# Kernel optimization log

Measured on AMD Instinct MI355X. Metric: run time of the kernel, lower is better.

Reference implementation:

```python
import jax, jax.numpy as jnp
import numpy as np

D_MODEL = 2048
NUM_HEADS = 16
HEAD_DIM = D_MODEL // NUM_HEADS
BATCH = 2
SEQ = 2048
ROPE_BASE = 10000.0


def apply_rope(x, start_pos=0):
    # x: [B, H, S, D] ; standard rotate-half RoPE
    B, H, S, D = x.shape
    inv_freq = 1.0 / (ROPE_BASE ** (jnp.arange(0, D, 2, dtype=jnp.float32) / D))  # [D/2]
    pos = jnp.arange(start_pos, start_pos + S, dtype=jnp.float32)  # [S]
    ang = pos[:, None] * inv_freq[None, :]  # [S, D/2]
    cos = jnp.cos(ang).astype(x.dtype)
    sin = jnp.sin(ang).astype(x.dtype)
    x1, x2 = x[..., : D // 2], x[..., D // 2 :]
    return jnp.concatenate([x1 * cos - x2 * sin, x1 * sin + x2 * cos], axis=-1)


def setup_inputs() -> dict:
    key = jax.random.key(0)
    ks = jax.random.split(key, 9)
    s = 1.0 / np.sqrt(D_MODEL)
    inp = {
        "x": jax.random.normal(ks[0], (BATCH, SEQ, D_MODEL), dtype=jnp.float32),
        "mask": jnp.tril(jnp.ones((SEQ, SEQ), dtype=jnp.float32)),  # causal
        "Wq_w": jax.random.normal(ks[1], (D_MODEL, D_MODEL), dtype=jnp.float32) * s,
        "Wq_b": jax.random.normal(ks[2], (D_MODEL,), dtype=jnp.float32) * 0.01,
        "Wk_w": jax.random.normal(ks[3], (D_MODEL, D_MODEL), dtype=jnp.float32) * s,
        "Wk_b": jax.random.normal(ks[4], (D_MODEL,), dtype=jnp.float32) * 0.01,
        "Wv_w": jax.random.normal(ks[5], (D_MODEL, D_MODEL), dtype=jnp.float32) * s,
        "Wv_b": jax.random.normal(ks[6], (D_MODEL,), dtype=jnp.float32) * 0.01,
        "Wo_w": jax.random.normal(ks[7], (D_MODEL, D_MODEL), dtype=jnp.float32) * s,
        "Wo_b": jax.random.normal(ks[8], (D_MODEL,), dtype=jnp.float32) * 0.01,
    }
    return inp


def reference(x, mask, Wq_w, Wq_b, Wk_w, Wk_b, Wv_w, Wv_b, Wo_w, Wo_b):
    B, S, _ = x.shape
    # projections (torch Linear: y = x @ W.T + b)
    Q = x @ Wq_w.T + Wq_b
    K = x @ Wk_w.T + Wk_b
    V = x @ Wv_w.T + Wv_b
    # [B, H, S, D]
    Q = Q.reshape(B, S, NUM_HEADS, HEAD_DIM).transpose(0, 2, 1, 3)
    K = K.reshape(B, S, NUM_HEADS, HEAD_DIM).transpose(0, 2, 1, 3)
    V = V.reshape(B, S, NUM_HEADS, HEAD_DIM).transpose(0, 2, 1, 3)
    Q = apply_rope(Q, start_pos=0)
    K = apply_rope(K, start_pos=0)
    scores = jnp.einsum("bhqd,bhkd->bhqk", Q, K) / jnp.sqrt(
        jnp.asarray(HEAD_DIM, dtype=x.dtype)
    )
    # 2-D mask -> broadcast over batch/head; masked_fill(mask==0, -inf)
    scores = jnp.where(mask[None, None, :S, :S] == 0, -jnp.inf, scores)
    attn = jax.nn.softmax(scores, axis=-1)
    out = jnp.einsum("bhqk,bhkd->bhqd", attn, V)
    out = out.transpose(0, 2, 1, 3).reshape(B, S, D_MODEL)
    return out @ Wo_w.T + Wo_b
```

## Files before the change

kernel.cpp:

```cpp
#include <hip/hip_runtime.h>
#include <math.h>

#define D_MODEL 2048
#define NHEADS  16
#define HDIM    128
#define BATCH   2
#define SEQ     2048
#define MTOT    (BATCH*SEQ)

typedef unsigned short u16;
typedef unsigned int   u32;
typedef __attribute__((ext_vector_type(8))) short  short8;
typedef __attribute__((ext_vector_type(8))) u16    ushort8;
typedef __attribute__((ext_vector_type(4))) u16    us4;
typedef __attribute__((ext_vector_type(4))) float  floatx4;

__device__ __forceinline__ u16 f2b(float f) {
    u32 u = __float_as_uint(f);
    return (u16)((u + 0x7fffu + ((u >> 16) & 1u)) >> 16);
}
__device__ __forceinline__ float b2f(u16 b) {
    return __uint_as_float(((u32)b) << 16);
}
__device__ __forceinline__ void async16(void* lds, const void* g) {
    __builtin_amdgcn_global_load_lds(
        (const __attribute__((address_space(1))) u32*)g,
        (__attribute__((address_space(3))) u32*)lds, 16, 0, 0);
}

__global__ __launch_bounds__(256)
void f2b_kernel(const float* __restrict__ x,
                const float* __restrict__ wq, const float* __restrict__ wk,
                const float* __restrict__ wv, const float* __restrict__ wo,
                u16* __restrict__ xb, u16* __restrict__ wqb, u16* __restrict__ wkb,
                u16* __restrict__ wvb, u16* __restrict__ wob)
{
    const int bid = blockIdx.x;
    const float* src; u16* dst; int lb;
    if (bid < 4096) { src = x; dst = xb; lb = bid; }
    else {
        const int t = (bid - 4096) >> 11;
        lb = (bid - 4096) & 2047;
        src = (t == 0) ? wq : (t == 1) ? wk : (t == 2) ? wv : wo;
        dst = (t == 0) ? wqb : (t == 1) ? wkb : (t == 2) ? wvb : wob;
    }
    const size_t e = ((size_t)lb * 256 + threadIdx.x) * 8;
    const float4 a = *(const float4*)&src[e];
    const float4 b = *(const float4*)&src[e + 4];
    union { u16 u[8]; uint4 v; } o;
    o.u[0] = f2b(a.x); o.u[1] = f2b(a.y); o.u[2] = f2b(a.z); o.u[3] = f2b(a.w);
    o.u[4] = f2b(b.x); o.u[5] = f2b(b.y); o.u[6] = f2b(b.z); o.u[7] = f2b(b.w);
    *(uint4*)&dst[e] = o.v;
}

__global__ __launch_bounds__(256)
void gemm_bf16(const u16* __restrict__ A,
               const u16* W0, const u16* W1, const u16* W2,
               const float* b0, const float* b1, const float* b2,
               void* C0, void* C1, void* C2, int mode)
{
    __shared__ __align__(16) u16 As[128 * 32];
    __shared__ __align__(16) u16 Bs[128 * 32];

    const int z = blockIdx.z;
    const u16*   W    = (z == 0) ? W0 : (z == 1) ? W1 : W2;
    const float* bias = (z == 0) ? b0 : (z == 1) ? b1 : b2;
    void*        C    = (z == 0) ? C0 : (z == 1) ? C1 : C2;

    const int tid  = threadIdx.x;
    const int lane = tid & 63;
    const int wv   = tid >> 6;
    const int wr   = wv >> 1, wc = wv & 1;
    const int m0 = blockIdx.y * 128, n0 = blockIdx.x * 128;

    floatx4 acc[4][4];
    #pragma unroll
    for (int i = 0; i < 4; ++i)
        #pragma unroll
        for (int j = 0; j < 4; ++j) acc[i][j] = (floatx4){0.f, 0.f, 0.f, 0.f};

    const int f0 = tid, f1 = tid + 256;
    const char* Ag = (const char*)(A + (size_t)m0 * 2048);
    const char* Wg = (const char*)(W + (size_t)n0 * 2048);
    const size_t a0 = (size_t)(f0 >> 2) * 4096 + (f0 & 3) * 16;
    const size_t a1 = (size_t)(f1 >> 2) * 4096 + (f1 & 3) * 16;

    const int lrow = lane & 15, lk = (lane >> 4) * 8;

    for (int k0 = 0; k0 < 2048; k0 += 32) {
        __syncthreads();
        const size_t kb = (size_t)k0 * 2;
        async16(&As[f0 * 8], Ag + a0 + kb);
        async16(&As[f1 * 8], Ag + a1 + kb);
        async16(&Bs[f0 * 8], Wg + a0 + kb);
        async16(&Bs[f1 * 8], Wg + a1 + kb);
        __syncthreads();

        short8 af[4], bf[4];
        #pragma unroll
        for (int i = 0; i < 4; ++i)
            af[i] = *(const short8*)&As[(wr * 64 + i * 16 + lrow) * 32 + lk];
        #pragma unroll
        for (int j = 0; j < 4; ++j)
            bf[j] = *(const short8*)&Bs[(wc * 64 + j * 16 + lrow) * 32 + lk];
        #pragma unroll
        for (int i = 0; i < 4; ++i)
            #pragma unroll
            for (int j = 0; j < 4; ++j)
                acc[i][j] = __builtin_amdgcn_mfma_f32_16x16x32_bf16(af[i], bf[j], acc[i][j], 0, 0, 0);
    }

    float bb[4];
    #pragma unroll
    for (int j = 0; j < 4; ++j) bb[j] = bias[n0 + wc * 64 + j * 16 + lrow];

    #pragma unroll
    for (int i = 0; i < 4; ++i) {
        #pragma unroll
        for (int j = 0; j < 4; ++j) {
            const int col  = n0 + wc * 64 + j * 16 + lrow;
            const int row0 = m0 + wr * 64 + i * 16 + (lane >> 4) * 4;
            if (mode == 0) {
                const int b = row0 >> 11, s = row0 & (SEQ - 1);
                const int h = col >> 7,  d = col & 127;
                if (z == 2) {
                    us4 pk;
                    #pragma unroll
                    for (int q = 0; q < 4; ++q) pk[q] = f2b(acc[i][j][q] + bb[j]);
                    *(us4*)&((u16*)C)[(((size_t)(b * NHEADS + h)) * HDIM + d) * SEQ + s] = pk;
                } else {
                    #pragma unroll
                    for (int q = 0; q < 4; ++q)
                        ((u16*)C)[(((size_t)(b * NHEADS + h)) * SEQ + s + q) * HDIM + d]
                            = f2b(acc[i][j][q] + bb[j]);
                }
            } else {
                #pragma unroll
                for (int q = 0; q < 4; ++q)
                    ((float*)C)[(size_t)(row0 + q) * D_MODEL + col] = acc[i][j][q] + bb[j];
            }
        }
    }
}

__global__ void rope_table(float* __restrict__ tcos, float* __restrict__ tsin)
{
    const int idx = blockIdx.x * 256 + threadIdx.x;
    const int s = idx >> 6, i = idx & 63;
    const float inv = powf(10000.0f, -(float)i / 64.0f);
    const float ang = (float)s * inv;
    tcos[idx] = cosf(ang);
    tsin[idx] = sinf(ang);
}

__global__ void rope_apply(u16* __restrict__ Q, u16* __restrict__ K,
                           const float* __restrict__ tcos, const float* __restrict__ tsin)
{
    const int idx = blockIdx.x * 256 + threadIdx.x;
    u16* P = blockIdx.y ? K : Q;
    const float sc = blockIdx.y ? 1.0f : 0.08838834764831845f;
    const int i   = idx & 63;
    const int bhs = idx >> 6;
    const int s   = bhs & (SEQ - 1);
    const size_t base = (size_t)bhs * HDIM;
    const float x1 = b2f(P[base + i]), x2 = b2f(P[base + i + 64]);
    const float c  = tcos[(s << 6) + i], sn = tsin[(s << 6) + i];
    P[base + i]      = f2b((x1 * c  - x2 * sn) * sc);
    P[base + i + 64] = f2b((x1 * sn + x2 * c) * sc);
}

__global__ __launch_bounds__(256, 2)
void flash_attn_mfma(const u16* __restrict__ Q, const u16* __restrict__ K,
                     const u16* __restrict__ Vt, u16* __restrict__ O)
{
    __shared__ __align__(16) u16 Ks[2][64 * 128];
    __shared__ __align__(16) u16 Vs[2][128 * 64];
    __shared__ __align__(16) u16 Ps[128 * 64];

    const int tid = threadIdx.x, lane = tid & 63, w = tid >> 6;
    const int l15 = lane & 15, l4 = lane >> 4;
    const int bh = blockIdx.y;
    const int qt = 15 - blockIdx.x;
    const int q0 = qt * 128;
    const int qw = q0 + w * 32;
    const size_t baseQK = (size_t)bh * SEQ * HDIM;
    const size_t baseV  = (size_t)bh * HDIM * SEQ;

    short8 qf[2][4];
    #pragma unroll
    for (int u = 0; u < 2; ++u) {
        const u16* Qg = Q + baseQK + (size_t)(qw + u * 16 + l15) * HDIM;
        #pragma unroll
        for (int kk = 0; kk < 4; ++kk) qf[u][kk] = *(const short8*)&Qg[kk * 32 + l4 * 8];
    }

    floatx4 o_acc[2][8];
    #pragma unroll
    for (int u = 0; u < 2; ++u)
        #pragma unroll
        for (int j2 = 0; j2 < 8; ++j2) o_acc[u][j2] = (floatx4){0.f, 0.f, 0.f, 0.f};
    float m_run[2] = {-INFINITY, -INFINITY}, l_run[2] = {0.f, 0.f};

    const int nt = 2 * qt + 2;

    #define STAGE(buf, k0_)                                                     \
    {                                                                           \
        const u16* Kg = K  + baseQK + (size_t)(k0_) * HDIM;                     \
        const u16* Vg = Vt + baseV  + (k0_);                                    \
        _Pragma("unroll")                                                       \
        for (int p_ = 0; p_ < 4; ++p_) {                                        \
            const int idx = p_ * 256 + tid;                                     \
            const int r_ = idx >> 4, c_ = idx & 15;                             \
            const int srcK = (c_ & 8) | ((c_ & 7) ^ (r_ & 7));                  \
            async16(&Ks[buf][idx * 8], Kg + r_ * HDIM + srcK * 8);              \
            const int rv = idx >> 3, cv = idx & 7;                              \
            const int srcV = cv ^ (rv & 7);                                     \
            async16(&Vs[buf][idx * 8], Vg + (size_t)rv * SEQ + srcV * 8);       \
        }                                                                       \
    }

    STAGE(0, 0);
    __syncthreads();
    int cur = 0;

    for (int t = 0; t < nt; ++t) {
        if (t + 1 < nt) STAGE(cur ^ 1, (t + 1) * 64);

        floatx4 s[2][4];
        #pragma unroll
        for (int u = 0; u < 2; ++u)
            #pragma unroll
            for (int j = 0; j < 4; ++j) s[u][j] = (floatx4){0.f, 0.f, 0.f, 0.f};
        #pragma unroll
        for (int j = 0; j < 4; ++j) {
            const int row = j * 16 + l15;
            #pragma unroll
            for (int kk = 0; kk < 4; ++kk) {
                const int x  = kk * 4 + l4;
                const int ch = (x & 8) | ((x & 7) ^ (row & 7));
                const short8 kf = *(const short8*)&Ks[cur][row * 128 + ch * 8];
                s[0][j] = __builtin_amdgcn_mfma_f32_16x16x32_bf16(kf, qf[0][kk], s[0][j], 0, 0, 0);
                s[1][j] = __builtin_amdgcn_mfma_f32_16x16x32_bf16(kf, qf[1][kk], s[1][j], 0, 0, 0);
            }
        }

        if (t >= nt - 2) {
            const int k0 = t * 64;
            #pragma unroll
            for (int u = 0; u < 2; ++u) {
                const int qg = qw + u * 16 + l15;
                #pragma unroll
                for (int j = 0; j < 4; ++j)
                    #pragma unroll
                    for (int r = 0; r < 4; ++r)
                        if (k0 + j * 16 + l4 * 4 + r > qg) s[u][j][r] = -INFINITY;
            }
        }

        float al[2];
        #pragma unroll
        for (int u = 0; u < 2; ++u) {
            float m0_ = fmaxf(fmaxf(s[u][0][0], s[u][0][1]), fmaxf(s[u][0][2], s[u][0][3]));
            float m1_ = fmaxf(fmaxf(s[u][1][0], s[u][1][1]), fmaxf(s[u][1][2], s[u][1][3]));
            float m2_ = fmaxf(fmaxf(s[u][2][0], s[u][2][1]), fmaxf(s[u][2][2], s[u][2][3]));
            float m3_ = fmaxf(fmaxf(s[u][3][0], s[u][3][1]), fmaxf(s[u][3][2], s[u][3][3]));
            float mt = fmaxf(fmaxf(m0_, m1_), fmaxf(m2_, m3_));
            mt = fmaxf(mt, __shfl_xor(mt, 16));
            mt = fmaxf(mt, __shfl_xor(mt, 32));
            const float mn = fmaxf(m_run[u], mt);
            al[u] = __expf(m_run[u] - mn);
            m_run[u] = mn;
            const int prow = w * 32 + u * 16 + l15;
            const int swz  = (prow & 7) << 3;
            float rs = 0.f;
            #pragma unroll
            for (int j = 0; j < 4; ++j) {
                float p0 = __expf(s[u][j][0] - mn), p1 = __expf(s[u][j][1] - mn);
                float p2 = __expf(s[u][j][2] - mn), p3 = __expf(s[u][j][3] - mn);
                rs += (p0 + p1) + (p2 + p3);
                us4 pk; pk[0] = f2b(p0); pk[1] = f2b(p1); pk[2] = f2b(p2); pk[3] = f2b(p3);
                *(us4*)&Ps[prow * 64 + ((j * 16 + l4 * 4) ^ swz)] = pk;
            }
            rs += __shfl_xor(rs, 16);
            rs += __shfl_xor(rs, 32);
            l_run[u] = l_run[u] * al[u] + rs;
        }

        #pragma unroll
        for (int u = 0; u < 2; ++u) {
            float alr[4];
            #pragma unroll
            for (int r = 0; r < 4; ++r) alr[r] = __shfl(al[u], l4 * 4 + r, 16);
            #pragma unroll
            for (int j2 = 0; j2 < 8; ++j2)
                #pragma unroll
                for (int r = 0; r < 4; ++r) o_acc[u][j2][r] *= alr[r];
        }

        #pragma unroll
        for (int ks = 0; ks < 2; ++ks) {
            short8 pf[2];
            #pragma unroll
            for (int u = 0; u < 2; ++u) {
                const int prow = w * 32 + u * 16 + l15;
                pf[u] = *(const short8*)&Ps[prow * 64 + ((ks * 32 + l4 * 8) ^ ((prow & 7) << 3))];
            }
            #pragma unroll
            for (int j2 = 0; j2 < 8; ++j2) {
                const int vrow = j2 * 16 + l15;
                const int vch  = (ks * 4 + l4) ^ (vrow & 7);
                const short8 vf = *(const short8*)&Vs[cur][vrow * 64 + vch * 8];
                o_acc[0][j2] = __builtin_amdgcn_mfma_f32_16x16x32_bf16(pf[0], vf, o_acc[0][j2], 0, 0, 0);
                o_acc[1][j2] = __builtin_amdgcn_mfma_f32_16x16x32_bf16(pf[1], vf, o_acc[1][j2], 0, 0, 0);
            }
        }

        __syncthreads();
        cur ^= 1;
    }

    const int b = bh >> 4, h = bh & 15;
    #pragma unroll
    for (int u = 0; u < 2; ++u) {
        const float invl = 1.f / l_run[u];
        float invr[4];
        #pragma unroll
        for (int r = 0; r < 4; ++r) invr[r] = __shfl(invl, l4 * 4 + r, 16);
        #pragma unroll
        for (int r = 0; r < 4; ++r) {
            const int s_ = qw + u * 16 + l4 * 4 + r;
            u16* dst = O + ((size_t)b * SEQ + s_) * D_MODEL + h * HDIM;
            #pragma unroll
            for (int j2 = 0; j2 < 8; ++j2)
                dst[j2 * 16 + l15] = f2b(o_acc[u][j2][r] * invr[r]);
        }
    }
    #undef STAGE
}

extern "C" void kernel_launch(void* const* d_in, const int* in_sizes, int n_in,
                              void* d_out, int out_size, void* d_ws, size_t ws_size,
                              hipStream_t stream)
{
    const float* x  = (const float*)d_in[0];
    const float* Wq = (const float*)d_in[2];
    const float* bq = (const float*)d_in[3];
    const float* Wk = (const float*)d_in[4];
    const float* bk = (const float*)d_in[5];
    const float* Wv = (const float*)d_in[6];
    const float* bv = (const float*)d_in[7];
    const float* Wo = (const float*)d_in[8];
    const float* bo = (const float*)d_in[9];
    float* out = (float*)d_out;

    const size_t TEN = (size_t)MTOT * D_MODEL;
    const size_t WEL = (size_t)D_MODEL * D_MODEL;
    char* p = (char*)d_ws;
    u16* xb  = (u16*)p; p += TEN * 2;
    u16* wqb = (u16*)p; p += WEL * 2;
    u16* wkb = (u16*)p; p += WEL * 2;
    u16* wvb = (u16*)p; p += WEL * 2;
    u16* wob = (u16*)p; p += WEL * 2;
    u16* Qb  = (u16*)p; p += TEN * 2;
    u16* Kb  = (u16*)p; p += TEN * 2;
    u16* Vb  = (u16*)p; p += TEN * 2;
    u16* An  = (u16*)p; p += TEN * 2;
    float* tc = (float*)p; p += (size_t)SEQ * 64 * 4;
    float* ts = (float*)p;

    f2b_kernel<<<dim3(12288), 256, 0, stream>>>(x, Wq, Wk, Wv, Wo,
                                                xb, wqb, wkb, wvb, wob);
    rope_table<<<dim3(512), 256, 0, stream>>>(tc, ts);
    gemm_bf16<<<dim3(16, 32, 3), 256, 0, stream>>>(xb, wqb, wkb, wvb,
                                                   bq, bk, bv, Qb, Kb, Vb, 0);
    rope_apply<<<dim3(16384, 2), 256, 0, stream>>>(Qb, Kb, tc, ts);
    flash_attn_mfma<<<dim3(16, 32), 256, 0, stream>>>(Qb, Kb, Vb, An);
    gemm_bf16<<<dim3(16, 32, 1), 256, 0, stream>>>(An, wob, wob, wob,
                                                   bo, bo, bo, out, out, out, 1);
}
```

Before: 457.3 us.

## Replace projection GEMM with pipelined 128x256 swizzled-LDS kernel and fused QKV launch

Replaces the single-buffered 128x128x32 GEMM with a 512-thread kernel using 128x256 tiles, a K step of 64 and double-buffered async loads. Loads are interleaved between MFMA sub-blocks, with XOR-swizzled LDS layouts and a block-index swizzle for L2 locality. The Q/K/V projections now run as one N=6144 GEMM over the contiguous weight buffers, with the bias and output tensor chosen per column. It also raises wave priority around the MFMA sections in flash attention. In exchange it uses much more LDS per block and hand-written waitcnt accounting, which limits occupancy and is fragile if the load count changes.

```diff
diff --git a/kernel.cpp b/kernel.cpp
--- a/kernel.cpp
+++ b/kernel.cpp
@@ -53,94 +53,121 @@
     *(uint4*)&dst[e] = o.v;
 }
 
-__global__ __launch_bounds__(256)
-void gemm_bf16(const u16* __restrict__ A,
-               const u16* W0, const u16* W1, const u16* W2,
-               const float* b0, const float* b1, const float* b2,
-               void* C0, void* C1, void* C2, int mode)
-{
-    __shared__ __align__(16) u16 As[128 * 32];
-    __shared__ __align__(16) u16 Bs[128 * 32];
-
-    const int z = blockIdx.z;
-    const u16*   W    = (z == 0) ? W0 : (z == 1) ? W1 : W2;
-    const float* bias = (z == 0) ? b0 : (z == 1) ? b1 : b2;
-    void*        C    = (z == 0) ? C0 : (z == 1) ? C1 : C2;
-
-    const int tid  = threadIdx.x;
-    const int lane = tid & 63;
-    const int wv   = tid >> 6;
-    const int wr   = wv >> 1, wc = wv & 1;
-    const int m0 = blockIdx.y * 128, n0 = blockIdx.x * 128;
-
-    floatx4 acc[4][4];
+__global__ __launch_bounds__(512, 2)
+void gemm8(const u16* __restrict__ A, const u16* __restrict__ W,
+           const float* __restrict__ bq, const float* __restrict__ bk,
+           const float* __restrict__ bv,
+           u16* __restrict__ Qb, u16* __restrict__ Kb, u16* __restrict__ Vb,
+           float* __restrict__ Cf, int mode)
+{
+    __shared__ __align__(16) u16 As[2][128 * 64];
+    __shared__ __align__(16) u16 Bs[2][256 * 64];
+
+    const int tid = threadIdx.x, lane = tid & 63, wn = tid >> 6;
+    const int l15 = lane & 15, l4 = lane >> 4;
+    const int cpx = (int)gridDim.x >> 3;
+    const int swz = ((int)blockIdx.x & 7) * cpx + ((int)blockIdx.x >> 3);
+    const int bm = swz & 31, bn = swz >> 5;
+    const int m0 = bm * 128, n0 = bn * 256;
+
+    const u16* Ag = A + (size_t)m0 * 2048;
+    const u16* Wg = W + (size_t)n0 * 2048;
+    const int lc = tid >> 3, ch = tid & 7;
+
+    #define STA(buf, kt, mq_) {                                                 \
+        const int row_ = (mq_) * 64 + lc;                                       \
+        const int cs_ = ch ^ (row_ & 7);                                        \
+        async16(&As[buf][row_ * 64 + ch * 8],                                   \
+                Ag + (size_t)row_ * 2048 + (kt) * 64 + cs_ * 8); }
+    #define STB(buf, kt, nsub) {                                               \
+        _Pragma("unroll") for (int r_ = 0; r_ < 2; ++r_) {                      \
+            const int col_ = (nsub) * 16 + (lc & 15) + (lc >> 4) * 32 + r_ * 128;\
+            const int cs_ = ch ^ (col_ & 7);                                    \
+            async16(&Bs[buf][col_ * 64 + ch * 8],                               \
+                    Wg + (size_t)col_ * 2048 + (kt) * 64 + cs_ * 8); } }
+
+    floatx4 acc[8][2];
     #pragma unroll
-    for (int i = 0; i < 4; ++i)
-        #pragma unroll
-        for (int j = 0; j < 4; ++j) acc[i][j] = (floatx4){0.f, 0.f, 0.f, 0.f};
-
-    const int f0 = tid, f1 = tid + 256;
-    const char* Ag = (const char*)(A + (size_t)m0 * 2048);
-    const char* Wg = (const char*)(W + (size_t)n0 * 2048);
-    const size_t a0 = (size_t)(f0 >> 2) * 4096 + (f0 & 3) * 16;
-    const size_t a1 = (size_t)(f1 >> 2) * 4096 + (f1 & 3) * 16;
-
-    const int lrow = lane & 15, lk = (lane >> 4) * 8;
-
-    for (int k0 = 0; k0 < 2048; k0 += 32) {
-        __syncthreads();
-        const size_t kb = (size_t)k0 * 2;
-        async16(&As[f0 * 8], Ag + a0 + kb);
-        async16(&As[f1 * 8], Ag + a1 + kb);
-        async16(&Bs[f0 * 8], Wg + a0 + kb);
-        async16(&Bs[f1 * 8], Wg + a1 + kb);
-        __syncthreads();
-
-        short8 af[4], bf[4];
-        #pragma unroll
-        for (int i = 0; i < 4; ++i)
-            af[i] = *(const short8*)&As[(wr * 64 + i * 16 + lrow) * 32 + lk];
-        #pragma unroll
-        for (int j = 0; j < 4; ++j)
-            bf[j] = *(const short8*)&Bs[(wc * 64 + j * 16 + lrow) * 32 + lk];
-        #pragma unroll
-        for (int i = 0; i < 4; ++i)
-            #pragma unroll
-            for (int j = 0; j < 4; ++j)
-                acc[i][j] = __builtin_amdgcn_mfma_f32_16x16x32_bf16(af[i], bf[j], acc[i][j], 0, 0, 0);
-    }
-
-    float bb[4];
+    for (int i = 0; i < 8; ++i)
+        #pragma unroll
+        for (int j = 0; j < 2; ++j) acc[i][j] = (floatx4){0.f, 0.f, 0.f, 0.f};
+
+    short8 af[4][2], bf[2][2];
+
+    #define LDA(mq_, buf) _Pragma("unroll") for (int i_ = 0; i_ < 4; ++i_) {    \
+        const int row_ = (mq_) * 64 + i_ * 16 + l15;                            \
+        _Pragma("unroll") for (int kk_ = 0; kk_ < 2; ++kk_) {                   \
+            const int c_ = (kk_ * 4 + l4) ^ (row_ & 7);                         \
+            af[i_][kk_] = *(const short8*)&As[buf][row_ * 64 + c_ * 8]; } }
+    #define LDB(nq_, buf) {                                                     \
+        const int col_ = wn * 32 + (nq_) * 16 + l15;                            \
+        _Pragma("unroll") for (int kk_ = 0; kk_ < 2; ++kk_) {                   \
+            const int c_ = (kk_ * 4 + l4) ^ (col_ & 7);                         \
+            bf[nq_][kk_] = *(const short8*)&Bs[buf][col_ * 64 + c_ * 8]; } }
+    #define MM(mq_, nq_) {                                                      \
+        __builtin_amdgcn_s_setprio(1);                                          \
+        _Pragma("unroll") for (int i_ = 0; i_ < 4; ++i_)                        \
+        _Pragma("unroll") for (int kk_ = 0; kk_ < 2; ++kk_)                     \
+            acc[(mq_) * 4 + i_][nq_] = __builtin_amdgcn_mfma_f32_16x16x32_bf16( \
+                af[i_][kk_], bf[nq_][kk_], acc[(mq_) * 4 + i_][nq_], 0, 0, 0);  \
+        __builtin_amdgcn_s_setprio(0);                                          \
+        __builtin_amdgcn_s_barrier(); }
+
+    STA(0, 0, 0); STB(0, 0, 0); STA(0, 0, 1); STB(0, 0, 1);
+    STA(1, 1, 0); STB(1, 1, 0);
+
+    #pragma unroll 2
+    for (int t = 0; t < 32; ++t) {
+        const int b = t & 1;
+        if (t < 31) { asm volatile("s_waitcnt vmcnt(3)" ::: "memory"); }
+        else        { asm volatile("s_waitcnt vmcnt(0)" ::: "memory"); }
+        __builtin_amdgcn_s_barrier();
+        if (t < 31) STA(b ^ 1, t + 1, 1);
+        LDA(0, b); LDB(0, b); MM(0, 0);
+        if (t < 31) STB(b ^ 1, t + 1, 1);
+        LDB(1, b); MM(0, 1);
+        if (t < 30) STA(b, t + 2, 0);
+        LDA(1, b); MM(1, 0);
+        if (t < 30) STB(b, t + 2, 0);
+        MM(1, 1);
+    }
+
     #pragma unroll
-    for (int j = 0; j < 4; ++j) bb[j] = bias[n0 + wc * 64 + j * 16 + lrow];
-
-    #pragma unroll
-    for (int i = 0; i < 4; ++i) {
-        #pragma unroll
-        for (int j = 0; j < 4; ++j) {
-            const int col  = n0 + wc * 64 + j * 16 + lrow;
-            const int row0 = m0 + wr * 64 + i * 16 + (lane >> 4) * 4;
+    for (int fm = 0; fm < 8; ++fm) {
+        #pragma unroll
+        for (int fn = 0; fn < 2; ++fn) {
+            const int col = n0 + wn * 32 + fn * 16 + l15;
+            const int row0 = m0 + fm * 16 + l4 * 4;
             if (mode == 0) {
-                const int b = row0 >> 11, s = row0 & (SEQ - 1);
-                const int h = col >> 7,  d = col & 127;
+                const int z = col >> 11, c = col & 2047;
+                const int h = c >> 7, d = c & 127;
+                const float bb = (z == 0 ? bq : z == 1 ? bk : bv)[c];
+                const int b_ = row0 >> 11, s = row0 & (SEQ - 1);
                 if (z == 2) {
                     us4 pk;
                     #pragma unroll
-                    for (int q = 0; q < 4; ++q) pk[q] = f2b(acc[i][j][q] + bb[j]);
-                    *(us4*)&((u16*)C)[(((size_t)(b * NHEADS + h)) * HDIM + d) * SEQ + s] = pk;
+                    for (int q = 0; q < 4; ++q) pk[q] = f2b(acc[fm][fn][q] + bb);
+                    *(us4*)&Vb[(((size_t)(b_ * NHEADS + h)) * HDIM + d) * SEQ + s] = pk;
                 } else {
+                    u16* dst = (z ? Kb : Qb);
                     #pragma unroll
                     for (int q = 0; q < 4; ++q)
-                        ((u16*)C)[(((size_t)(b * NHEADS + h)) * SEQ + s + q) * HDIM + d]
-                            = f2b(acc[i][j][q] + bb[j]);
+                        dst[(((size_t)(b_ * NHEADS + h)) * SEQ + s + q) * HDIM + d]
+                            = f2b(acc[fm][fn][q] + bb);
                 }
             } else {
+                const float bb = bq[col];
                 #pragma unroll
                 for (int q = 0; q < 4; ++q)
-                    ((float*)C)[(size_t)(row0 + q) * D_MODEL + col] = acc[i][j][q] + bb[j];
-            }
-        }
-    }
+                    Cf[(size_t)(row0 + q) * D_MODEL + col] = acc[fm][fn][q] + bb;
+            }
+        }
+    }
+    #undef STA
+    #undef STB
+    #undef LDA
+    #undef LDB
+    #undef MM
 }
 
 __global__ void rope_table(float* __restrict__ tcos, float* __restrict__ tsin)
@@ -231,6 +258,7 @@
         for (int u = 0; u < 2; ++u)
             #pragma unroll
             for (int j = 0; j < 4; ++j) s[u][j] = (floatx4){0.f, 0.f, 0.f, 0.f};
+        __builtin_amdgcn_s_setprio(1);
         #pragma unroll
         for (int j = 0; j < 4; ++j) {
             const int row = j * 16 + l15;
@@ -243,6 +271,7 @@
                 s[1][j] = __builtin_amdgcn_mfma_f32_16x16x32_bf16(kf, qf[1][kk], s[1][j], 0, 0, 0);
             }
         }
+        __builtin_amdgcn_s_setprio(0);
 
         if (t >= nt - 2) {
             const int k0 = t * 64;
@@ -271,7 +300,7 @@
             al[u] = __expf(m_run[u] - mn);
             m_run[u] = mn;
             const int prow = w * 32 + u * 16 + l15;
-            const int swz  = (prow & 7) << 3;
+            const int swzp = (prow & 7) << 3;
             float rs = 0.f;
             #pragma unroll
             for (int j = 0; j < 4; ++j) {
@@ -279,7 +308,7 @@
                 float p2 = __expf(s[u][j][2] - mn), p3 = __expf(s[u][j][3] - mn);
                 rs += (p0 + p1) + (p2 + p3);
                 us4 pk; pk[0] = f2b(p0); pk[1] = f2b(p1); pk[2] = f2b(p2); pk[3] = f2b(p3);
-                *(us4*)&Ps[prow * 64 + ((j * 16 + l4 * 4) ^ swz)] = pk;
+                *(us4*)&Ps[prow * 64 + ((j * 16 + l4 * 4) ^ swzp)] = pk;
             }
             rs += __shfl_xor(rs, 16);
             rs += __shfl_xor(rs, 32);
@@ -297,6 +326,7 @@
                 for (int r = 0; r < 4; ++r) o_acc[u][j2][r] *= alr[r];
         }
 
+        __builtin_amdgcn_s_setprio(1);
         #pragma unroll
         for (int ks = 0; ks < 2; ++ks) {
             short8 pf[2];
@@ -314,6 +344,7 @@
                 o_acc[1][j2] = __builtin_amdgcn_mfma_f32_16x16x32_bf16(pf[1], vf, o_acc[1][j2], 0, 0, 0);
             }
         }
+        __builtin_amdgcn_s_setprio(0);
 
         __syncthreads();
         cur ^= 1;
@@ -371,10 +402,10 @@
     f2b_kernel<<<dim3(12288), 256, 0, stream>>>(x, Wq, Wk, Wv, Wo,
                                                 xb, wqb, wkb, wvb, wob);
     rope_table<<<dim3(512), 256, 0, stream>>>(tc, ts);
-    gemm_bf16<<<dim3(16, 32, 3), 256, 0, stream>>>(xb, wqb, wkb, wvb,
-                                                   bq, bk, bv, Qb, Kb, Vb, 0);
+    gemm8<<<dim3(768), 512, 0, stream>>>(xb, wqb, bq, bk, bv,
+                                         Qb, Kb, Vb, nullptr, 0);
     rope_apply<<<dim3(16384, 2), 256, 0, stream>>>(Qb, Kb, tc, ts);
     flash_attn_mfma<<<dim3(16, 32), 256, 0, stream>>>(Qb, Kb, Vb, An);
-    gemm_bf16<<<dim3(16, 32, 1), 256, 0, stream>>>(An, wob, wob, wob,
-                                                   bo, bo, bo, out, out, out, 1);
-}
+    gemm8<<<dim3(256), 512, 0, stream>>>(An, wob, bo, bo, bo,
+                                         nullptr, nullptr, nullptr, out, 1);
+}
```

After: 493.0 us. 7.8% more time.
